# Performance work log

Measured on AMD Instinct MI355X. Metric: run time of the kernel, lower is better.

The kernel has to match this reference:

```python
import jax, jax.numpy as jnp
import numpy as np

B, T, C, H = 16, 512, 1080, 20  # batch, seq, embd, heads; head_dim = C // H = 54

def setup_inputs() -> dict:
    key = jax.random.key(0)
    k1, k2, k3, k4, k5 = jax.random.split(key, 5)
    s = 0.02
    return {
        "x": jax.random.normal(k1, (B, T, C), dtype=jnp.float32),
        "W_attn": jax.random.normal(k2, (C, 3 * C), dtype=jnp.float32) * s,
        "b_attn": jax.random.normal(k3, (3 * C,), dtype=jnp.float32) * s,
        "W_proj": jax.random.normal(k4, (C, C), dtype=jnp.float32) * s,
        "b_proj": jax.random.normal(k5, (C,), dtype=jnp.float32) * s,
    }

def reference(x, W_attn, b_attn, W_proj, b_proj):
    Bb, Tt, Cc = x.shape
    hd = Cc // H
    qkv = jnp.einsum('btc,cd->btd', x, W_attn) + b_attn  # [B,T,3C]
    q, k, v = jnp.split(qkv, 3, axis=2)
    # [B,T,C] -> [B,H,T,hd]
    q = q.reshape(Bb, Tt, H, hd).transpose(0, 2, 1, 3)
    k = k.reshape(Bb, Tt, H, hd).transpose(0, 2, 1, 3)
    v = v.reshape(Bb, Tt, H, hd).transpose(0, 2, 1, 3)
    att = jnp.einsum('bhqd,bhkd->bhqk', q, k) * (1.0 / jnp.sqrt(jnp.float32(hd)))
    causal = jnp.tril(jnp.ones((Tt, Tt), dtype=bool))
    att = jnp.where(causal, att, -jnp.inf)
    att = jax.nn.softmax(att, axis=-1)
    y = jnp.einsum('bhqk,bhkd->bhqd', att, v)  # [B,H,T,hd]
    y = y.transpose(0, 2, 1, 3).reshape(Bb, Tt, Cc)
    return jnp.einsum('btc,cd->btd', y, W_proj) + b_proj
```

## Files before the change

### kernel.cpp

```cpp
#include <hip/hip_runtime.h>
#include <hip/hip_bf16.h>

#define B_   16
#define T_   512
#define C_   1080
#define H_   20
#define HD_  54
#define DP_  64
#define M_   (B_ * T_)
#define KP_  1088
#define NT_  17
#define NQKV_ 3840
#define NPRJ_ 1152
#define NBT_ (B_ * H_ * T_)

typedef short bf16x8 __attribute__((ext_vector_type(8)));
typedef float f32x4  __attribute__((ext_vector_type(4)));
typedef unsigned short u16x8 __attribute__((ext_vector_type(8)));

__device__ __forceinline__ void gload_lds16(const void* g, void* l) {
    __builtin_amdgcn_global_load_lds(
        (const __attribute__((address_space(1))) void*)g,
        (__attribute__((address_space(3))) void*)l,
        16, 0, 0);
}

__device__ __forceinline__ unsigned short f2b(float x) {
    return __builtin_bit_cast(unsigned short, __float2bfloat16(x));
}

__global__ __launch_bounds__(256) void cvt_pad(
    const float* __restrict__ src, __hip_bfloat16* __restrict__ dst)
{
    int idx = blockIdx.x * 256 + threadIdx.x;
    if (idx >= M_ * (KP_ / 4)) return;
    int m = idx / (KP_ / 4), c = idx - m * (KP_ / 4);
    ushort4 o;
    if (c < C_ / 4) {
        float4 v = *reinterpret_cast<const float4*>(src + (size_t)m * C_ + c * 4);
        o.x = f2b(v.x); o.y = f2b(v.y); o.z = f2b(v.z); o.w = f2b(v.w);
    } else {
        o.x = o.y = o.z = o.w = 0;
    }
    *reinterpret_cast<ushort4*>(reinterpret_cast<unsigned short*>(dst) + (size_t)m * KP_ + c * 4) = o;
}

__global__ __launch_bounds__(256) void prep(
    const float* __restrict__ W_attn, const float* __restrict__ W_proj,
    const float* __restrict__ b_attn,
    __hip_bfloat16* __restrict__ wta, __hip_bfloat16* __restrict__ wtp,
    float* __restrict__ bp)
{
    __shared__ float tile[32][33];
    const int bx = blockIdx.x, by = blockIdx.y;
    const int tx = threadIdx.x & 31, ty = threadIdx.x >> 5;

    if (bx < 120) {
        int n0 = bx * 32, k0 = by * 32;
        int np = n0 + tx;
        int which = np / 1280;
        int rem = np - which * 1280;
        int h = rem >> 6, d = rem & 63;
        int sn = which * C_ + h * HD_ + d;
        bool valid = d < HD_;
        #pragma unroll
        for (int i = 0; i < 32; i += 8) {
            int k = k0 + ty + i;
            tile[ty + i][tx] = (valid && k < C_) ? W_attn[(size_t)k * (3 * C_) + sn] : 0.f;
        }
        __syncthreads();
        #pragma unroll
        for (int i = 0; i < 32; i += 8) {
            int n = n0 + ty + i, k = k0 + tx;
            wta[(size_t)n * KP_ + k] = __float2bfloat16(tile[tx][ty + i]);
        }
    } else if (bx < 156) {
        int n0 = (bx - 120) * 32, k0 = by * 32;
        #pragma unroll
        for (int i = 0; i < 32; i += 8) {
            int k = k0 + ty + i, n = n0 + tx;
            tile[ty + i][tx] = (k < C_ && n < C_) ? W_proj[(size_t)k * C_ + n] : 0.f;
        }
        __syncthreads();
        #pragma unroll
        for (int i = 0; i < 32; i += 8) {
            int n = n0 + ty + i, k = k0 + tx;
            wtp[(size_t)n * KP_ + k] = __float2bfloat16(tile[tx][ty + i]);
        }
    } else if (by == 0) {
        int i = (bx - 156) * 256 + threadIdx.x;
        if (i < NQKV_) {
            int which = i / 1280, rem = i - which * 1280;
            int h = rem >> 6, d = rem & 63;
            float v = (d < HD_) ? b_attn[which * C_ + h * HD_ + d] : 0.f;
            if (which == 2 && d == 63) v = 1.0f;
            bp[i] = v;
        }
    }
}

__global__ __launch_bounds__(512, 2) void gemm256(
    const unsigned short* __restrict__ A,
    const unsigned short* __restrict__ Bt,
    const float* __restrict__ bias,
    unsigned short* __restrict__ outQ,
    unsigned short* __restrict__ outK,
    unsigned short* __restrict__ outV)
{
    __shared__ __align__(16) char smem[131072];

    const int tid  = threadIdx.x;
    const int lane = tid & 63;
    const int wv   = tid >> 6;
    const int wr   = wv >> 2;
    const int wc   = wv & 3;
    const int lq   = lane & 15;
    const int lg   = lane >> 4;

    const int id  = blockIdx.y * 15 + blockIdx.x;
    const int xcd = id & 7;
    const int j   = id >> 3;
    const int m0  = (xcd * 4 + (j & 3)) * 256;
    const int n0  = (j >> 2) * 256;

    unsigned gA[2], gB[2];
    const int ld0 = tid * 16, ld1 = tid * 16 + 8192;
    #pragma unroll
    for (int i = 0; i < 2; ++i) {
        int ci = tid + i * 512;
        int r  = ci >> 3;
        int kc = (ci & 7) ^ (r & 7);
        gA[i] = (unsigned)(m0 + r) * KP_ + kc * 8;
        gB[i] = (unsigned)(n0 + r) * KP_ + kc * 8;
    }
    const unsigned HALFSTEP = 128u * KP_;

    auto stage = [&](int buf, int hIdx, unsigned k0) {
        char* sb = smem + buf * 65536 +
                   (hIdx < 2 ? hIdx * 16384 : 32768 + (hIdx - 2) * 16384);
        const unsigned short* sp = (hIdx < 2) ? A : Bt;
        unsigned extra = (hIdx & 1) ? HALFSTEP : 0u;
        gload_lds16(sp + ((hIdx < 2) ? gA[0] : gB[0]) + extra + k0, sb + ld0);
        gload_lds16(sp + ((hIdx < 2) ? gA[1] : gB[1]) + extra + k0, sb + ld1);
    };

    const int s0 = (lg ^ (lq & 7)) * 16;
    const int s1 = ((4 + lg) ^ (lq & 7)) * 16;
    const int aBase = wr * 16384 + lq * 128;
    const int bBase = 32768 + (wc >> 1) * 16384 + (wc & 1) * 8192 + lq * 128;

    f32x4 acc[8][4] = {};

    stage(0, 0, 0); stage(0, 1, 0); stage(0, 2, 0); stage(0, 3, 0);

    for (int t = 0; t < NT_; ++t) {
        const int cur = t & 1;
        if (t + 1 < NT_) {
            const int nb = cur ^ 1;
            const unsigned k0n = (unsigned)(t + 1) * 64;
            stage(nb, 0, k0n); stage(nb, 1, k0n); stage(nb, 2, k0n); stage(nb, 3, k0n);
            asm volatile("s_waitcnt vmcnt(8)" ::: "memory");
        } else {
            asm volatile("s_waitcnt vmcnt(0)" ::: "memory");
        }
        __builtin_amdgcn_s_barrier();

        const char* Ab = smem + cur * 65536 + aBase;
        const char* Bb = smem + cur * 65536 + bBase;

        bf16x8 bfr[4][2];
        #pragma unroll
        for (int ni = 0; ni < 4; ++ni) {
            bfr[ni][0] = *reinterpret_cast<const bf16x8*>(Bb + ni * 2048 + s0);
            bfr[ni][1] = *reinterpret_cast<const bf16x8*>(Bb + ni * 2048 + s1);
        }
        bf16x8 afA[2][2], afB[2][2];
        #pragma unroll
        for (int i = 0; i < 2; ++i) {
            afA[0][i] = *reinterpret_cast<const bf16x8*>(Ab + i * 2048 + s0);
            afA[1][i] = *reinterpret_cast<const bf16x8*>(Ab + i * 2048 + s1);
        }
        __builtin_amdgcn_s_setprio(1);
        #pragma unroll
        for (int q = 0; q < 4; ++q) {
            if (q < 3) {
                #pragma unroll
                for (int i = 0; i < 2; ++i) {
                    if (q & 1) {
                        afA[0][i] = *reinterpret_cast<const bf16x8*>(Ab + ((q + 1) * 2 + i) * 2048 + s0);
                        afA[1][i] = *reinterpret_cast<const bf16x8*>(Ab + ((q + 1) * 2 + i) * 2048 + s1);
                    } else {
                        afB[0][i] = *reinterpret_cast<const bf16x8*>(Ab + ((q + 1) * 2 + i) * 2048 + s0);
                        afB[1][i] = *reinterpret_cast<const bf16x8*>(Ab + ((q + 1) * 2 + i) * 2048 + s1);
                    }
                }
            }
            #pragma unroll
            for (int kk = 0; kk < 2; ++kk)
                #pragma unroll
                for (int i = 0; i < 2; ++i)
                    #pragma unroll
                    for (int ni = 0; ni < 4; ++ni)
                        acc[q * 2 + i][ni] = __builtin_amdgcn_mfma_f32_16x16x32_bf16(
                            (q & 1) ? afB[kk][i] : afA[kk][i], bfr[ni][kk],
                            acc[q * 2 + i][ni], 0, 0, 0);
        }
        __builtin_amdgcn_s_setprio(0);
        __builtin_amdgcn_s_barrier();
    }

    const int which = n0 / 1280;
    if (which < 2) {
        unsigned short* dst = which ? outK : outQ;
        #pragma unroll
        for (int mi = 0; mi < 8; ++mi) {
            int mg = m0 + wr * 128 + mi * 16 + lg * 4;
            int b = mg >> 9, t0 = mg & (T_ - 1);
            #pragma unroll
            for (int ni = 0; ni < 4; ++ni) {
                int nl = wc * 64 + ni * 16 + lq;
                int ng = n0 + nl - which * 1280;
                int h = ng >> 6, d = ng & 63;
                float bs = bias[n0 + nl];
                size_t basei = ((size_t)(b * H_ + h) * T_ + t0) * DP_ + d;
                #pragma unroll
                for (int j2 = 0; j2 < 4; ++j2)
                    dst[basei + (size_t)j2 * DP_] = f2b(acc[mi][ni][j2] + bs);
            }
        }
    } else {
        unsigned short* lt = (unsigned short*)smem;
        #pragma unroll
        for (int hm = 0; hm < 2; ++hm) {
            if (hm == 1) __syncthreads();
            if (wr == hm) {
                #pragma unroll
                for (int mi = 0; mi < 8; ++mi) {
                    int ml = mi * 16 + lg * 4;
                    int mc = ml >> 3, mo = ml & 7;
                    #pragma unroll
                    for (int ni = 0; ni < 4; ++ni) {
                        int nl = wc * 64 + ni * 16 + lq;
                        float bs = bias[n0 + nl];
                        ushort4 pk;
                        pk.x = f2b(acc[mi][ni][0] + bs);
                        pk.y = f2b(acc[mi][ni][1] + bs);
                        pk.z = f2b(acc[mi][ni][2] + bs);
                        pk.w = f2b(acc[mi][ni][3] + bs);
                        int slot = mc ^ ((nl >> 3) & 15);
                        *reinterpret_cast<ushort4*>(lt + nl * 136 + slot * 8 + mo) = pk;
                    }
                }
            }
            __syncthreads();
            #pragma unroll
            for (int it = 0; it < 8; ++it) {
                int idx = it * 512 + tid;
                int c2 = idx >> 4, j2 = idx & 15;
                int slot = j2 ^ ((c2 >> 3) & 15);
                u16x8 v = *reinterpret_cast<const u16x8*>(lt + c2 * 136 + slot * 8);
                int ng = n0 + c2 - 2560;
                int h = ng >> 6, d = ng & 63;
                int mg = m0 + hm * 128 + j2 * 8;
                int b = mg >> 9, t = mg & (T_ - 1);
                *reinterpret_cast<u16x8*>(outV + ((size_t)(b * H_ + h) * DP_ + d) * T_ + t) = v;
            }
        }
    }
}

__global__ __launch_bounds__(256) void gemm_mfma_p(
    const unsigned short* __restrict__ A,
    const unsigned short* __restrict__ Bt,
    const float* __restrict__ bias,
    float* __restrict__ outP)
{
    __shared__ __align__(16) char smem[65536];

    const int tid  = threadIdx.x;
    const int lane = tid & 63;
    const int wv   = tid >> 6;
    const int wm   = (wv >> 1) * 64;
    const int wn   = (wv & 1) * 64;
    const int lr   = lane & 15;
    const int lk   = lane >> 4;

    const int gx  = gridDim.x;
    const int gy  = gridDim.y;
    const int id  = blockIdx.y * gx + blockIdx.x;
    const int xcd = id & 7;
    const int j   = id >> 3;
    const int mpc = gy >> 3;
    const int m0  = (xcd * mpc + j % mpc) * 128;
    const int n0  = (j / mpc) * 128;

    unsigned aOff[4], bOff[4];
    int ciB[4];
    #pragma unroll
    for (int it = 0; it < 4; ++it) {
        int ci = it * 256 + tid;
        int r = ci >> 3, p = ci & 7;
        int kc = p ^ (r & 7);
        aOff[it] = (unsigned)(m0 + r) * KP_ + kc * 8;
        bOff[it] = (unsigned)(n0 + r) * KP_ + kc * 8;
        ciB[it] = ci * 16;
    }
    int aRd[2][4], bRd[2][4];
    #pragma unroll
    for (int kk = 0; kk < 2; ++kk) {
        #pragma unroll
        for (int mi = 0; mi < 4; ++mi) {
            int row = wm + mi * 16 + lr;
            aRd[kk][mi] = row * 128 + ((kk * 4 + lk) ^ (row & 7)) * 16;
            int rowb = wn + mi * 16 + lr;
            bRd[kk][mi] = 16384 + rowb * 128 + ((kk * 4 + lk) ^ (rowb & 7)) * 16;
        }
    }

    f32x4 acc[4][4] = {};

    auto stage = [&](int buf, int kt) {
        const unsigned k0 = kt * 64;
        char* sb = smem + buf * 32768;
        #pragma unroll
        for (int it = 0; it < 4; ++it)
            gload_lds16(A + aOff[it] + k0, sb + ciB[it]);
        #pragma unroll
        for (int it = 0; it < 4; ++it)
            gload_lds16(Bt + bOff[it] + k0, sb + 16384 + ciB[it]);
    };

    stage(0, 0);
    for (int kt = 0; kt < NT_; ++kt) {
        const int c = kt & 1;
        if (kt + 1 < NT_) {
            stage(1 - c, kt + 1);
            asm volatile("s_waitcnt vmcnt(8)" ::: "memory");
        } else {
            asm volatile("s_waitcnt vmcnt(0)" ::: "memory");
        }
        __builtin_amdgcn_s_barrier();
        asm volatile("" ::: "memory");

        const char* base = smem + c * 32768;
        #pragma unroll
        for (int kk = 0; kk < 2; ++kk) {
            bf16x8 af[4], bfr[4];
            #pragma unroll
            for (int mi = 0; mi < 4; ++mi)
                af[mi] = *reinterpret_cast<const bf16x8*>(base + aRd[kk][mi]);
            #pragma unroll
            for (int ni = 0; ni < 4; ++ni)
                bfr[ni] = *reinterpret_cast<const bf16x8*>(base + bRd[kk][ni]);
            #pragma unroll
            for (int mi = 0; mi < 4; ++mi)
                #pragma unroll
                for (int ni = 0; ni < 4; ++ni)
                    acc[mi][ni] = __builtin_amdgcn_mfma_f32_16x16x32_bf16(
                        af[mi], bfr[ni], acc[mi][ni], 0, 0, 0);
        }
        asm volatile("" ::: "memory");
        __builtin_amdgcn_s_barrier();
    }

    #pragma unroll
    for (int mi = 0; mi < 4; ++mi) {
        int mrow = m0 + wm + mi * 16 + lk * 4;
        #pragma unroll
        for (int ni = 0; ni < 4; ++ni) {
            int n = n0 + wn + ni * 16 + lr;
            if (n < C_) {
                float bs = bias[n];
                #pragma unroll
                for (int j2 = 0; j2 < 4; ++j2)
                    outP[(size_t)(mrow + j2) * C_ + n] = acc[mi][ni][j2] + bs;
            }
        }
    }
}

__global__ __launch_bounds__(256) void attn_mfma(
    const unsigned short* __restrict__ Q, const unsigned short* __restrict__ K,
    const unsigned short* __restrict__ Vt, __hip_bfloat16* __restrict__ Y)
{
    __shared__ __align__(16) char kvs[16384];
    __shared__ __align__(16) unsigned short ps[4][16][72];

    const int tid  = threadIdx.x;
    const int lane = tid & 63;
    const int wv   = tid >> 6;
    const int lq   = lane & 15;
    const int lg   = lane >> 4;
    const int bh   = blockIdx.y;
    const int qt   = blockIdx.x;
    const int qbase = qt * 64;
    const float cs = 0.13608276348795434f * 1.44269504f;

    bf16x8 qf[2];
    {
        const unsigned short* qp = Q + ((size_t)bh * T_ + qbase + wv * 16 + lq) * DP_;
        qf[0] = *reinterpret_cast<const bf16x8*>(qp + lg * 8);
        qf[1] = *reinterpret_cast<const bf16x8*>(qp + 32 + lg * 8);
    }

    unsigned kOff[2], vOff[2];
    int ciB[2];
    #pragma unroll
    for (int it = 0; it < 2; ++it) {
        int ci = it * 256 + tid;
        int r = ci >> 3, p = ci & 7;
        int pc = p ^ (r & 7);
        kOff[it] = (unsigned)(r * DP_ + pc * 8);
        vOff[it] = (unsigned)(r * T_ + pc * 8);
        ciB[it] = ci * 16;
    }
    const unsigned short* Kb = K  + (size_t)bh * T_ * DP_;
    const unsigned short* Vb = Vt + (size_t)bh * DP_ * T_;

    f32x4 o[4] = {};
    unsigned short* pbase = &ps[wv][0][0];
    const int nt = qt + 1;

    for (int kt = 0; kt < nt; ++kt) {
        const int kbase = kt * 64;
        #pragma unroll
        for (int it = 0; it < 2; ++it)
            gload_lds16(Kb + kOff[it] + (unsigned)kbase * DP_, kvs + ciB[it]);
        #pragma unroll
        for (int it = 0; it < 2; ++it)
            gload_lds16(Vb + vOff[it] + (unsigned)kbase, kvs + 8192 + ciB[it]);
        __syncthreads();

        f32x4 s[4] = {};
        #pragma unroll
        for (int dc = 0; dc < 2; ++dc) {
            #pragma unroll
            for (int ni = 0; ni < 4; ++ni) {
                int row = ni * 16 + lq;
                int ch  = (dc * 4 + lg) ^ (row & 7);
                bf16x8 kf = *reinterpret_cast<const bf16x8*>(kvs + row * 128 + ch * 16);
                s[ni] = __builtin_amdgcn_mfma_f32_16x16x32_bf16(qf[dc], kf, s[ni], 0, 0, 0);
            }
        }

        if (kt == qt) {
            #pragma unroll
            for (int ni = 0; ni < 4; ++ni) {
                int kg = kbase + ni * 16 + lq;
                #pragma unroll
                for (int j = 0; j < 4; ++j) {
                    int qg = qbase + wv * 16 + lg * 4 + j;
                    s[ni][j] = (kg > qg) ? -3.0e38f : s[ni][j];
                }
            }
        }
        #pragma unroll
        for (int ni = 0; ni < 4; ++ni) {
            #pragma unroll
            for (int j = 0; j < 4; ++j) {
                float p = exp2f(s[ni][j] * cs);
                int qr = lg * 4 + j;
                int cidx = (ni * 2 + (lq >> 3)) ^ (qr & 7);
                pbase[qr * 72 + cidx * 8 + (lq & 7)] = f2b(p);
            }
        }

        asm volatile("s_waitcnt lgkmcnt(0)" ::: "memory");
        __builtin_amdgcn_sched_barrier(0);

        #pragma unroll
        for (int dc = 0; dc < 2; ++dc) {
            int cc = (dc * 4 + lg) ^ (lq & 7);
            bf16x8 pf = *reinterpret_cast<const bf16x8*>(pbase + lq * 72 + cc * 8);
            #pragma unroll
            for (int ni = 0; ni < 4; ++ni) {
                int row = ni * 16 + lq;
                int ch  = (dc * 4 + lg) ^ (row & 7);
                bf16x8 vf = *reinterpret_cast<const bf16x8*>(kvs + 8192 + row * 128 + ch * 16);
                o[ni] = __builtin_amdgcn_mfma_f32_16x16x32_bf16(pf, vf, o[ni], 0, 0, 0);
            }
        }
        __syncthreads();
    }

    const int b = bh / H_, h = bh - b * H_;
    #pragma unroll
    for (int j = 0; j < 4; ++j) {
        float l = __shfl(o[3][j], (lane & 48) | 15, 64);
        float inv = 1.f / l;
        int t = qbase + wv * 16 + lg * 4 + j;
        #pragma unroll
        for (int ni = 0; ni < 4; ++ni) {
            int d = ni * 16 + lq;
            if (d < HD_)
                Y[((size_t)b * T_ + t) * KP_ + h * HD_ + d] =
                    __float2bfloat16(o[ni][j] * inv);
        }
    }
}

extern "C" void kernel_launch(void* const* d_in, const int* in_sizes, int n_in,
                              void* d_out, int out_size, void* d_ws, size_t ws_size,
                              hipStream_t stream)
{
    const float* x      = (const float*)d_in[0];
    const float* W_attn = (const float*)d_in[1];
    const float* b_attn = (const float*)d_in[2];
    const float* W_proj = (const float*)d_in[3];
    const float* b_proj = (const float*)d_in[4];
    float* out = (float*)d_out;

    __hip_bfloat16* xb = (__hip_bfloat16*)d_ws;
    unsigned short* qb = (unsigned short*)(xb + (size_t)M_ * KP_);
    unsigned short* kb = qb + (size_t)NBT_ * DP_;
    unsigned short* vtb = kb + (size_t)NBT_ * DP_;
    __hip_bfloat16* wta = (__hip_bfloat16*)(vtb + (size_t)NBT_ * DP_);
    __hip_bfloat16* wtp = wta + (size_t)NQKV_ * KP_;
    float* bp = (float*)(wtp + (size_t)NPRJ_ * KP_);
    __hip_bfloat16* yb = xb;

    cvt_pad<<<(M_ * (KP_ / 4) + 255) / 256, 256, 0, stream>>>(x, xb);
    prep<<<dim3(171, 34), 256, 0, stream>>>(W_attn, W_proj, b_attn, wta, wtp, bp);

    gemm256<<<dim3(NQKV_ / 256, M_ / 256), 512, 0, stream>>>(
        (const unsigned short*)xb, (const unsigned short*)wta, bp,
        qb, kb, vtb);

    attn_mfma<<<dim3(T_ / 64, B_ * H_), 256, 0, stream>>>(qb, kb, vtb, yb);

    gemm_mfma_p<<<dim3(NPRJ_ / 128, M_ / 128), 256, 0, stream>>>(
        (const unsigned short*)yb, (const unsigned short*)wtp, b_proj, out);
}
```

Measured before the change: 182.7 us.

## Share K/V tiles across two query tiles per attention block and merge prep kernels

```diff
diff --git a/kernel.cpp b/kernel.cpp
--- a/kernel.cpp
+++ b/kernel.cpp
@@ -29,33 +29,38 @@
     return __builtin_bit_cast(unsigned short, __float2bfloat16(x));
 }
 
-__global__ __launch_bounds__(256) void cvt_pad(
-    const float* __restrict__ src, __hip_bfloat16* __restrict__ dst)
-{
-    int idx = blockIdx.x * 256 + threadIdx.x;
-    if (idx >= M_ * (KP_ / 4)) return;
-    int m = idx / (KP_ / 4), c = idx - m * (KP_ / 4);
-    ushort4 o;
-    if (c < C_ / 4) {
-        float4 v = *reinterpret_cast<const float4*>(src + (size_t)m * C_ + c * 4);
-        o.x = f2b(v.x); o.y = f2b(v.y); o.z = f2b(v.z); o.w = f2b(v.w);
-    } else {
-        o.x = o.y = o.z = o.w = 0;
-    }
-    *reinterpret_cast<ushort4*>(reinterpret_cast<unsigned short*>(dst) + (size_t)m * KP_ + c * 4) = o;
-}
-
-__global__ __launch_bounds__(256) void prep(
-    const float* __restrict__ W_attn, const float* __restrict__ W_proj,
-    const float* __restrict__ b_attn,
+#define PB_CVT  8704
+#define PB_WTA  4080
+#define PB_WTP  1224
+__global__ __launch_bounds__(256) void prep_all(
+    const float* __restrict__ x, const float* __restrict__ W_attn,
+    const float* __restrict__ W_proj, const float* __restrict__ b_attn,
+    __hip_bfloat16* __restrict__ xb,
     __hip_bfloat16* __restrict__ wta, __hip_bfloat16* __restrict__ wtp,
     float* __restrict__ bp)
 {
     __shared__ float tile[32][33];
-    const int bx = blockIdx.x, by = blockIdx.y;
+    int id = blockIdx.x;
+
+    if (id < PB_CVT) {
+        int idx = id * 256 + threadIdx.x;
+        int m = idx / (KP_ / 4), c = idx - m * (KP_ / 4);
+        ushort4 o;
+        if (c < C_ / 4) {
+            float4 v = *reinterpret_cast<const float4*>(x + (size_t)m * C_ + c * 4);
+            o.x = f2b(v.x); o.y = f2b(v.y); o.z = f2b(v.z); o.w = f2b(v.w);
+        } else {
+            o.x = o.y = o.z = o.w = 0;
+        }
+        *reinterpret_cast<ushort4*>(reinterpret_cast<unsigned short*>(xb) +
+                                    (size_t)m * KP_ + c * 4) = o;
+        return;
+    }
+    id -= PB_CVT;
     const int tx = threadIdx.x & 31, ty = threadIdx.x >> 5;
 
-    if (bx < 120) {
+    if (id < PB_WTA) {
+        int bx = id % 120, by = id / 120;
         int n0 = bx * 32, k0 = by * 32;
         int np = n0 + tx;
         int which = np / 1280;
@@ -74,8 +79,13 @@
             int n = n0 + ty + i, k = k0 + tx;
             wta[(size_t)n * KP_ + k] = __float2bfloat16(tile[tx][ty + i]);
         }
-    } else if (bx < 156) {
-        int n0 = (bx - 120) * 32, k0 = by * 32;
+        return;
+    }
+    id -= PB_WTA;
+
+    if (id < PB_WTP) {
+        int bx = id % 36, by = id / 36;
+        int n0 = bx * 32, k0 = by * 32;
         #pragma unroll
         for (int i = 0; i < 32; i += 8) {
             int k = k0 + ty + i, n = n0 + tx;
@@ -87,8 +97,12 @@
             int n = n0 + ty + i, k = k0 + tx;
             wtp[(size_t)n * KP_ + k] = __float2bfloat16(tile[tx][ty + i]);
         }
-    } else if (by == 0) {
-        int i = (bx - 156) * 256 + threadIdx.x;
+        return;
+    }
+    id -= PB_WTP;
+
+    {
+        int i = id * 256 + threadIdx.x;
         if (i < NQKV_) {
             int which = i / 1280, rem = i - which * 1280;
             int h = rem >> 6, d = rem & 63;
@@ -379,106 +393,103 @@
     }
 }
 
-__global__ __launch_bounds__(256) void attn_mfma(
+__global__ __launch_bounds__(512) void attn_mfma(
     const unsigned short* __restrict__ Q, const unsigned short* __restrict__ K,
     const unsigned short* __restrict__ Vt, __hip_bfloat16* __restrict__ Y)
 {
     __shared__ __align__(16) char kvs[16384];
-    __shared__ __align__(16) unsigned short ps[4][16][72];
+    __shared__ __align__(16) unsigned short ps[8][16][72];
 
     const int tid  = threadIdx.x;
     const int lane = tid & 63;
     const int wv   = tid >> 6;
+    const int grp  = wv >> 2;
+    const int wq   = wv & 3;
     const int lq   = lane & 15;
     const int lg   = lane >> 4;
     const int bh   = blockIdx.y;
-    const int qt   = blockIdx.x;
-    const int qbase = qt * 64;
+    const int qt_own = blockIdx.x * 2 + grp;
+    const int qbase  = qt_own * 64;
     const float cs = 0.13608276348795434f * 1.44269504f;
 
     bf16x8 qf[2];
     {
-        const unsigned short* qp = Q + ((size_t)bh * T_ + qbase + wv * 16 + lq) * DP_;
+        const unsigned short* qp = Q + ((size_t)bh * T_ + qbase + wq * 16 + lq) * DP_;
         qf[0] = *reinterpret_cast<const bf16x8*>(qp + lg * 8);
         qf[1] = *reinterpret_cast<const bf16x8*>(qp + 32 + lg * 8);
     }
 
-    unsigned kOff[2], vOff[2];
-    int ciB[2];
-    #pragma unroll
-    for (int it = 0; it < 2; ++it) {
-        int ci = it * 256 + tid;
-        int r = ci >> 3, p = ci & 7;
-        int pc = p ^ (r & 7);
-        kOff[it] = (unsigned)(r * DP_ + pc * 8);
-        vOff[it] = (unsigned)(r * T_ + pc * 8);
-        ciB[it] = ci * 16;
-    }
+    const int sr = tid >> 3, sp = tid & 7;
+    const int spc = sp ^ (sr & 7);
+    const unsigned kOff = (unsigned)(sr * DP_ + spc * 8);
+    const unsigned vOff = (unsigned)(sr * T_ + spc * 8);
     const unsigned short* Kb = K  + (size_t)bh * T_ * DP_;
     const unsigned short* Vb = Vt + (size_t)bh * DP_ * T_;
 
     f32x4 o[4] = {};
     unsigned short* pbase = &ps[wv][0][0];
-    const int nt = qt + 1;
+    const int nt = blockIdx.x * 2 + 2;
 
     for (int kt = 0; kt < nt; ++kt) {
         const int kbase = kt * 64;
-        #pragma unroll
-        for (int it = 0; it < 2; ++it)
-            gload_lds16(Kb + kOff[it] + (unsigned)kbase * DP_, kvs + ciB[it]);
-        #pragma unroll
-        for (int it = 0; it < 2; ++it)
-            gload_lds16(Vb + vOff[it] + (unsigned)kbase, kvs + 8192 + ciB[it]);
+        gload_lds16(Kb + kOff + (unsigned)kbase * DP_, kvs + tid * 16);
+        gload_lds16(Vb + vOff + (unsigned)kbase, kvs + 8192 + tid * 16);
         __syncthreads();
 
-        f32x4 s[4] = {};
-        #pragma unroll
-        for (int dc = 0; dc < 2; ++dc) {
+        if (kt <= qt_own) {
+            f32x4 s[4] = {};
+            __builtin_amdgcn_s_setprio(1);
+            #pragma unroll
+            for (int dc = 0; dc < 2; ++dc) {
+                #pragma unroll
+                for (int ni = 0; ni < 4; ++ni) {
+                    int row = ni * 16 + lq;
+                    int ch  = (dc * 4 + lg) ^ (row & 7);
+                    bf16x8 kf = *reinterpret_cast<const bf16x8*>(kvs + row * 128 + ch * 16);
+                    s[ni] = __builtin_amdgcn_mfma_f32_16x16x32_bf16(qf[dc], kf, s[ni], 0, 0, 0);
+                }
+            }
+            __builtin_amdgcn_s_setprio(0);
+
+            if (kt == qt_own) {
+                #pragma unroll
+                for (int ni = 0; ni < 4; ++ni) {
+                    int kg = kbase + ni * 16 + lq;
+                    #pragma unroll
+                    for (int j = 0; j < 4; ++j) {
+                        int qg = qbase + wq * 16 + lg * 4 + j;
+                        s[ni][j] = (kg > qg) ? -3.0e38f : s[ni][j];
+                    }
+                }
+            }
             #pragma unroll
             for (int ni = 0; ni < 4; ++ni) {
-                int row = ni * 16 + lq;
-                int ch  = (dc * 4 + lg) ^ (row & 7);
-                bf16x8 kf = *reinterpret_cast<const bf16x8*>(kvs + row * 128 + ch * 16);
-                s[ni] = __builtin_amdgcn_mfma_f32_16x16x32_bf16(qf[dc], kf, s[ni], 0, 0, 0);
-            }
-        }
-
-        if (kt == qt) {
-            #pragma unroll
-            for (int ni = 0; ni < 4; ++ni) {
-                int kg = kbase + ni * 16 + lq;
                 #pragma unroll
                 for (int j = 0; j < 4; ++j) {
-                    int qg = qbase + wv * 16 + lg * 4 + j;
-                    s[ni][j] = (kg > qg) ? -3.0e38f : s[ni][j];
+                    float p = exp2f(s[ni][j] * cs);
+                    int qr = lg * 4 + j;
+                    int cidx = (ni * 2 + (lq >> 3)) ^ (qr & 7);
+                    pbase[qr * 72 + cidx * 8 + (lq & 7)] = f2b(p);
                 }
             }
-        }
-        #pragma unroll
-        for (int ni = 0; ni < 4; ++ni) {
-            #pragma unroll
-            for (int j = 0; j < 4; ++j) {
-                float p = exp2f(s[ni][j] * cs);
-                int qr = lg * 4 + j;
-                int cidx = (ni * 2 + (lq >> 3)) ^ (qr & 7);
-                pbase[qr * 72 + cidx * 8 + (lq & 7)] = f2b(p);
-            }
-        }
-
-        asm volatile("s_waitcnt lgkmcnt(0)" ::: "memory");
-        __builtin_amdgcn_sched_barrier(0);
-
-        #pragma unroll
-        for (int dc = 0; dc < 2; ++dc) {
-            int cc = (dc * 4 + lg) ^ (lq & 7);
-            bf16x8 pf = *reinterpret_cast<const bf16x8*>(pbase + lq * 72 + cc * 8);
-            #pragma unroll
-            for (int ni = 0; ni < 4; ++ni) {
-                int row = ni * 16 + lq;
-                int ch  = (dc * 4 + lg) ^ (row & 7);
-                bf16x8 vf = *reinterpret_cast<const bf16x8*>(kvs + 8192 + row * 128 + ch * 16);
-                o[ni] = __builtin_amdgcn_mfma_f32_16x16x32_bf16(pf, vf, o[ni], 0, 0, 0);
-            }
+
+            asm volatile("s_waitcnt lgkmcnt(0)" ::: "memory");
+            __builtin_amdgcn_sched_barrier(0);
+
+            __builtin_amdgcn_s_setprio(1);
+            #pragma unroll
+            for (int dc = 0; dc < 2; ++dc) {
+                int cc = (dc * 4 + lg) ^ (lq & 7);
+                bf16x8 pf = *reinterpret_cast<const bf16x8*>(pbase + lq * 72 + cc * 8);
+                #pragma unroll
+                for (int ni = 0; ni < 4; ++ni) {
+                    int row = ni * 16 + lq;
+                    int ch  = (dc * 4 + lg) ^ (row & 7);
+                    bf16x8 vf = *reinterpret_cast<const bf16x8*>(kvs + 8192 + row * 128 + ch * 16);
+                    o[ni] = __builtin_amdgcn_mfma_f32_16x16x32_bf16(pf, vf, o[ni], 0, 0, 0);
+                }
+            }
+            __builtin_amdgcn_s_setprio(0);
         }
         __syncthreads();
     }
@@ -488,7 +499,7 @@
     for (int j = 0; j < 4; ++j) {
         float l = __shfl(o[3][j], (lane & 48) | 15, 64);
         float inv = 1.f / l;
-        int t = qbase + wv * 16 + lg * 4 + j;
+        int t = qbase + wq * 16 + lg * 4 + j;
         #pragma unroll
         for (int ni = 0; ni < 4; ++ni) {
             int d = ni * 16 + lq;
@@ -519,14 +530,14 @@
     float* bp = (float*)(wtp + (size_t)NPRJ_ * KP_);
     __hip_bfloat16* yb = xb;
 
-    cvt_pad<<<(M_ * (KP_ / 4) + 255) / 256, 256, 0, stream>>>(x, xb);
-    prep<<<dim3(171, 34), 256, 0, stream>>>(W_attn, W_proj, b_attn, wta, wtp, bp);
+    prep_all<<<PB_CVT + PB_WTA + PB_WTP + 15, 256, 0, stream>>>(
+        x, W_attn, W_proj, b_attn, xb, wta, wtp, bp);
 
     gemm256<<<dim3(NQKV_ / 256, M_ / 256), 512, 0, stream>>>(
         (const unsigned short*)xb, (const unsigned short*)wta, bp,
         qb, kb, vtb);
 
-    attn_mfma<<<dim3(T_ / 64, B_ * H_), 256, 0, stream>>>(qb, kb, vtb, yb);
+    attn_mfma<<<dim3(T_ / 128, B_ * H_), 512, 0, stream>>>(qb, kb, vtb, yb);
 
     gemm_mfma_p<<<dim3(NPRJ_ / 128, M_ / 128), 256, 0, stream>>>(
         (const unsigned short*)yb, (const unsigned short*)wtp, b_proj, out);
```

Measured after the change: 169.2 us. 1.08x faster.
